# Performance work log

Measured on AMD Instinct MI355X. Metric: run time of the kernel, lower is better.

## Reference

```python
import jax, jax.numpy as jnp
import numpy as np

N_NODES = 50000
N_EDGES = 1600000
IN_DIM = 128
HIDDEN = 256
N_CLASSES = 2
N_GRAPHS = 512
BN_EPS = 1e-5


def setup_inputs() -> dict:
    key = jax.random.key(0)
    ks = jax.random.split(key, 12)
    x = jax.random.normal(ks[0], (N_NODES, IN_DIM), dtype=jnp.float32)
    edge_index = jax.random.randint(ks[1], (2, N_EDGES), 0, N_NODES, dtype=jnp.int64)
    batch = jnp.sort(jax.random.randint(ks[2], (N_NODES,), 0, N_GRAPHS, dtype=jnp.int64))
    s1 = 1.0 / np.sqrt(IN_DIM)
    s2 = 1.0 / np.sqrt(HIDDEN)
    return {
        "x": x,
        "edge_index": edge_index,
        "batch": batch,
        # GIN MLP: Linear(in,hidden) -> BN -> ReLU -> Linear(hidden,hidden)
        "W1": jax.random.uniform(ks[3], (IN_DIM, HIDDEN), jnp.float32, -s1, s1),
        "b1": jnp.zeros((HIDDEN,), jnp.float32),
        "g1": jnp.ones((HIDDEN,), jnp.float32),
        "be1": jnp.zeros((HIDDEN,), jnp.float32),
        "W2": jax.random.uniform(ks[4], (HIDDEN, HIDDEN), jnp.float32, -s2, s2),
        "b2": jnp.zeros((HIDDEN,), jnp.float32),
        # attention gate: Linear(hidden, 1)
        "Wg": jax.random.uniform(ks[5], (HIDDEN, 1), jnp.float32, -s2, s2),
        "bg": jnp.zeros((1,), jnp.float32),
        # head: BN(hidden) -> Dropout(eval: identity) -> Linear(hidden, n_classes)
        "g2": jnp.ones((HIDDEN,), jnp.float32),
        "be2": jnp.zeros((HIDDEN,), jnp.float32),
        "Wh": jax.random.uniform(ks[6], (HIDDEN, N_CLASSES), jnp.float32, -s2, s2),
        "bh": jnp.zeros((N_CLASSES,), jnp.float32),
    }


def _batchnorm(h, gamma, beta):
    # training-mode BN: batch statistics over axis 0 (biased variance, as torch)
    mu = jnp.mean(h, axis=0)
    var = jnp.mean(jnp.square(h - mu), axis=0)
    return gamma * (h - mu) * jax.lax.rsqrt(var + BN_EPS) + beta


def reference(x, edge_index, batch, W1, b1, g1, be1, W2, b2, Wg, bg, g2, be2, Wh, bh):
    src, dst = edge_index[0], edge_index[1]
    # GINConv (eps=0): agg_i = sum_{j->i} x_j ; h = MLP(x + agg)
    agg = jax.ops.segment_sum(x[src], dst, num_segments=N_NODES)  # [N, in_dim]
    h = x + agg
    h = h @ W1 + b1                      # [N, hidden]
    h = jax.nn.relu(_batchnorm(h, g1, be1))
    h = h @ W2 + b2                      # [N, hidden]
    h = jax.nn.relu(h)                   # outer F.relu in forward
    # AttentionalAggregation: segment softmax of gate, weighted sum per graph
    gate = h @ Wg + bg                   # [N, 1]
    m = jax.ops.segment_max(gate, batch, num_segments=N_GRAPHS)  # [G, 1]
    e = jnp.exp(gate - m[batch])
    s = jax.ops.segment_sum(e, batch, num_segments=N_GRAPHS)     # [G, 1]
    alpha = e / s[batch]                 # [N, 1]
    pooled = jax.ops.segment_sum(alpha * h, batch, num_segments=N_GRAPHS)  # [G, hidden]
    # head: BN -> (Dropout eval = identity) -> Linear -> log_softmax
    z = _batchnorm(pooled, g2, be2) @ Wh + bh  # [G, n_classes]
    return jax.nn.log_softmax(z, axis=-1)
```

## Files before the change

kernel.cpp:

```cpp
#include <hip/hip_runtime.h>

typedef unsigned int u32;
typedef unsigned short ushort_t;
typedef __attribute__((ext_vector_type(8))) short bf16x8;
typedef __attribute__((ext_vector_type(4))) float f32x4;

__device__ __forceinline__ float bf2f_lo(u32 u){
  union{u32 i; float f;} v; v.i = u<<16; return v.f;
}
__device__ __forceinline__ float bf2f_hi(u32 u){
  union{u32 i; float f;} v; v.i = u & 0xFFFF0000u; return v.f;
}
__device__ __forceinline__ float bf2f_s(ushort_t u){
  union{u32 i; float f;} v; v.i = ((u32)u)<<16; return v.f;
}
__device__ __forceinline__ u32 pack2bf(float a, float b){
  union{float f; u32 i;} va, vb; va.f=a; vb.f=b;
  u32 ra = (va.i + 0x7FFF + ((va.i>>16)&1)) >> 16;
  u32 rb = (vb.i + 0x7FFF + ((vb.i>>16)&1)) & 0xFFFF0000u;
  return ra | rb;
}
__device__ __forceinline__ ushort_t f2bf1(float f){
  union{float f; u32 i;} v; v.f=f;
  u32 r = v.i + 0x7FFF + ((v.i>>16)&1);
  return (ushort_t)(r>>16);
}

__global__ __launch_bounds__(256) void to_bf16(const float* __restrict__ x, u32* __restrict__ xb, long n4){
  long i = (long)blockIdx.x*256 + threadIdx.x;
  if(i*4 >= n4*4) return;
  float4 v = ((const float4*)x)[i];
  uint2 o; o.x = pack2bf(v.x, v.y); o.y = pack2bf(v.z, v.w);
  ((uint2*)xb)[i] = o;
}

__global__ __launch_bounds__(256) void transpose_w(const float* __restrict__ W, ushort_t* __restrict__ Wt, int K){
  int n = blockIdx.x;
  for(int k = threadIdx.x; k < K; k += 256){
    Wt[(size_t)n*K + k] = f2bf1(W[(size_t)k*256 + n]);
  }
}

__global__ __launch_bounds__(256) void hist_k(const int* __restrict__ dst, int* __restrict__ bcount,
                                              int E, int N, int NB){
  __shared__ int h[1024];
  for(int i=threadIdx.x; i<1024; i+=256) h[i]=0;
  __syncthreads();
  int e0 = blockIdx.x*8192;
  int e1 = min(e0+8192, E);
  for(int i=e0+threadIdx.x; i<e1; i+=256){
    int d = dst[i];
    if((u32)d >= (u32)N) d = 0;
    atomicAdd(&h[d>>6], 1);
  }
  __syncthreads();
  for(int i=threadIdx.x; i<NB; i+=256){
    int v = h[i];
    if(v) atomicAdd(&bcount[i], v);
  }
}

__global__ __launch_bounds__(256) void bucket_scan(const int* __restrict__ bcount, int* __restrict__ bstart,
                                                   int* __restrict__ bcursor, int NB){
  __shared__ int tsum[256];
  int t = threadIdx.x;
  int base = t*4;
  int a0 = (base+0<NB)?bcount[base+0]:0;
  int a1 = (base+1<NB)?bcount[base+1]:0;
  int a2 = (base+2<NB)?bcount[base+2]:0;
  int a3 = (base+3<NB)?bcount[base+3]:0;
  int s0=a0, s1=s0+a1, s2=s1+a2, s3=s2+a3;
  tsum[t]=s3; __syncthreads();
  #pragma unroll
  for(int d=1; d<256; d<<=1){
    int v = (t>=d)?tsum[t-d]:0;
    __syncthreads();
    tsum[t]+=v;
    __syncthreads();
  }
  int prev = (t>0)?tsum[t-1]:0;
  if(base+0<NB){ bstart[base+0]=prev;    bcursor[(base+0)*16]=0; }
  if(base+1<NB){ bstart[base+1]=prev+s0; bcursor[(base+1)*16]=0; }
  if(base+2<NB){ bstart[base+2]=prev+s1; bcursor[(base+2)*16]=0; }
  if(base+3<NB){ bstart[base+3]=prev+s2; bcursor[(base+3)*16]=0; }
  if(t==255){ bstart[NB]=prev+s3; }
}

__global__ __launch_bounds__(256) void binscatter2(const int* __restrict__ src, const int* __restrict__ dst,
                                                   const int* __restrict__ bstart, int* __restrict__ bcursor,
                                                   u32* __restrict__ pairs, int E, int N, int NB){
  __shared__ int hist[1024];
  __shared__ int base[1024];
  int e0 = blockIdx.x*8192;
  int e1 = min(e0+8192, E);
  for(int i=threadIdx.x; i<NB; i+=256) hist[i]=0;
  __syncthreads();
  for(int i=e0+threadIdx.x; i<e1; i+=256){
    int d = dst[i];
    if((u32)d >= (u32)N) d = 0;
    atomicAdd(&hist[d>>6], 1);
  }
  __syncthreads();
  for(int i=threadIdx.x; i<NB; i+=256){
    int c = hist[i];
    base[i] = c ? (bstart[i] + atomicAdd(&bcursor[i*16], c)) : 0;
    hist[i] = 0;
  }
  __syncthreads();
  for(int i=e0+threadIdx.x; i<e1; i+=256){
    int d = dst[i]; if((u32)d >= (u32)N) d = 0;
    int s = src[i]; if((u32)s >= (u32)N) s = 0;
    int b = d>>6;
    int loc = atomicAdd(&hist[b], 1);
    pairs[base[b]+loc] = (u32)s | (((u32)(d & 63))<<17);
  }
}

#define BCAP 4096
__global__ __launch_bounds__(512) void gather_bucket(const u32* __restrict__ xb,
                                                     const u32* __restrict__ pairs,
                                                     const int* __restrict__ bstart,
                                                     u32* __restrict__ h0b, int N){
  __shared__ int lsrc[BCAP];
  __shared__ int dcnt[64];
  __shared__ int dstart[65];
  __shared__ int dcur[64];
  int b = blockIdx.x;
  int p0 = bstart[b], p1 = bstart[b+1];
  int cnt = p1 - p0;
  int tid = threadIdx.x;
  if(tid < 64) dcnt[tid] = 0;
  __syncthreads();
  bool fits = (cnt <= BCAP) && (cnt >= 0);
  if(fits){
    for(int i=tid; i<cnt; i+=512){
      u32 u = pairs[p0+i];
      atomicAdd(&dcnt[(u>>17)&63], 1);
    }
    __syncthreads();
    if(tid==0){
      int run=0;
      #pragma unroll
      for(int j=0;j<64;j++){ dstart[j]=run; dcur[j]=run; run+=dcnt[j]; }
      dstart[64]=run;
    }
    __syncthreads();
    for(int i=tid; i<cnt; i+=512){
      u32 u = pairs[p0+i];
      int pos = atomicAdd(&dcur[(u>>17)&63], 1);
      lsrc[pos] = (int)(u & 0x1FFFFu);
    }
    __syncthreads();
  }
  const uint4* xr = (const uint4*)xb;
  int slot = tid >> 4;
  int c = tid & 15;
  for(int pass=0; pass<2; pass++){
    int r = pass*32 + slot;
    int node = b*64 + r;
    if(node >= N) continue;
    uint4 xv = xr[(size_t)node*16 + c];
    float acc[8] = {
      bf2f_lo(xv.x), bf2f_hi(xv.x), bf2f_lo(xv.y), bf2f_hi(xv.y),
      bf2f_lo(xv.z), bf2f_hi(xv.z), bf2f_lo(xv.w), bf2f_hi(xv.w) };
    if(fits){
      int ds = dstart[r], de = dstart[r+1];
      int j = ds;
      for(; j+8 <= de; j += 8){
        int s0=lsrc[j+0], s1=lsrc[j+1], s2=lsrc[j+2], s3=lsrc[j+3];
        int s4=lsrc[j+4], s5=lsrc[j+5], s6=lsrc[j+6], s7=lsrc[j+7];
        uint4 v0 = xr[(size_t)s0*16 + c];
        uint4 v1 = xr[(size_t)s1*16 + c];
        uint4 v2 = xr[(size_t)s2*16 + c];
        uint4 v3 = xr[(size_t)s3*16 + c];
        uint4 v4 = xr[(size_t)s4*16 + c];
        uint4 v5 = xr[(size_t)s5*16 + c];
        uint4 v6 = xr[(size_t)s6*16 + c];
        uint4 v7 = xr[(size_t)s7*16 + c];
        acc[0]+=bf2f_lo(v0.x)+bf2f_lo(v1.x)+bf2f_lo(v2.x)+bf2f_lo(v3.x)
               +bf2f_lo(v4.x)+bf2f_lo(v5.x)+bf2f_lo(v6.x)+bf2f_lo(v7.x);
        acc[1]+=bf2f_hi(v0.x)+bf2f_hi(v1.x)+bf2f_hi(v2.x)+bf2f_hi(v3.x)
               +bf2f_hi(v4.x)+bf2f_hi(v5.x)+bf2f_hi(v6.x)+bf2f_hi(v7.x);
        acc[2]+=bf2f_lo(v0.y)+bf2f_lo(v1.y)+bf2f_lo(v2.y)+bf2f_lo(v3.y)
               +bf2f_lo(v4.y)+bf2f_lo(v5.y)+bf2f_lo(v6.y)+bf2f_lo(v7.y);
        acc[3]+=bf2f_hi(v0.y)+bf2f_hi(v1.y)+bf2f_hi(v2.y)+bf2f_hi(v3.y)
               +bf2f_hi(v4.y)+bf2f_hi(v5.y)+bf2f_hi(v6.y)+bf2f_hi(v7.y);
        acc[4]+=bf2f_lo(v0.z)+bf2f_lo(v1.z)+bf2f_lo(v2.z)+bf2f_lo(v3.z)
               +bf2f_lo(v4.z)+bf2f_lo(v5.z)+bf2f_lo(v6.z)+bf2f_lo(v7.z);
        acc[5]+=bf2f_hi(v0.z)+bf2f_hi(v1.z)+bf2f_hi(v2.z)+bf2f_hi(v3.z)
               +bf2f_hi(v4.z)+bf2f_hi(v5.z)+bf2f_hi(v6.z)+bf2f_hi(v7.z);
        acc[6]+=bf2f_lo(v0.w)+bf2f_lo(v1.w)+bf2f_lo(v2.w)+bf2f_lo(v3.w)
               +bf2f_lo(v4.w)+bf2f_lo(v5.w)+bf2f_lo(v6.w)+bf2f_lo(v7.w);
        acc[7]+=bf2f_hi(v0.w)+bf2f_hi(v1.w)+bf2f_hi(v2.w)+bf2f_hi(v3.w)
               +bf2f_hi(v4.w)+bf2f_hi(v5.w)+bf2f_hi(v6.w)+bf2f_hi(v7.w);
      }
      for(; j < de; j++){
        int s = lsrc[j];
        uint4 v = xr[(size_t)s*16 + c];
        acc[0]+=bf2f_lo(v.x); acc[1]+=bf2f_hi(v.x);
        acc[2]+=bf2f_lo(v.y); acc[3]+=bf2f_hi(v.y);
        acc[4]+=bf2f_lo(v.z); acc[5]+=bf2f_hi(v.z);
        acc[6]+=bf2f_lo(v.w); acc[7]+=bf2f_hi(v.w);
      }
    } else {
      for(int i=0;i<cnt;i++){
        u32 u = pairs[p0+i];
        if((int)((u>>17)&63) == r){
          int s = (int)(u & 0x1FFFFu);
          uint4 v = xr[(size_t)s*16 + c];
          acc[0]+=bf2f_lo(v.x); acc[1]+=bf2f_hi(v.x);
          acc[2]+=bf2f_lo(v.y); acc[3]+=bf2f_hi(v.y);
          acc[4]+=bf2f_lo(v.z); acc[5]+=bf2f_hi(v.z);
          acc[6]+=bf2f_lo(v.w); acc[7]+=bf2f_hi(v.w);
        }
      }
    }
    uint4 o;
    o.x = pack2bf(acc[0],acc[1]); o.y = pack2bf(acc[2],acc[3]);
    o.z = pack2bf(acc[4],acc[5]); o.w = pack2bf(acc[6],acc[7]);
    ((uint4*)h0b)[(size_t)node*16 + c] = o;
  }
}

template<int K, bool BNA, bool RELUOUT, bool GATE, bool ABF16, bool OUTBF16>
__global__ __launch_bounds__(512) void gemm_mfma(const void* __restrict__ Ap, const ushort_t* __restrict__ Wt,
                                                 const float* __restrict__ bias,
                                                 const float* __restrict__ scale, const float* __restrict__ shift,
                                                 void* __restrict__ Cp, int M,
                                                 const float* __restrict__ Wg, const float* __restrict__ bg,
                                                 float* __restrict__ gate){
  __shared__ uint4 Al[8*129];
  __shared__ uint4 Bl[8*257];
  __shared__ float gacc[128];
  const int tid  = threadIdx.x;
  const int lane = tid & 63;
  const int wave = tid >> 6;
  const int lm   = lane & 15;
  const int q    = lane >> 4;
  const int mhalf= wave >> 2;
  const int nq   = wave & 3;
  const int m0   = blockIdx.x * 128;

  if(GATE && tid < 128) gacc[tid] = 0.f;

  f32x4 acc[4][4];
  #pragma unroll
  for(int i=0;i<4;i++)
    #pragma unroll
    for(int j=0;j<4;j++) acc[i][j] = (f32x4){0.f,0.f,0.f,0.f};

  for(int k0=0; k0<K; k0+=64){
    #pragma unroll
    for(int i=0;i<2;i++){
      int idx = tid*2 + i;
      int m = idx >> 3, c = idx & 7;
      int grow = m0 + m;
      int kk = k0 + c*8;
      uint4 v = make_uint4(0,0,0,0);
      if(ABF16){
        if(grow < M) v = *(const uint4*)((const ushort_t*)Ap + (size_t)grow*K + kk);
        if(BNA){
          float f0=bf2f_lo(v.x), f1=bf2f_hi(v.x), f2=bf2f_lo(v.y), f3=bf2f_hi(v.y);
          float f4=bf2f_lo(v.z), f5=bf2f_hi(v.z), f6=bf2f_lo(v.w), f7=bf2f_hi(v.w);
          float4 s0 = *(const float4*)(scale+kk),  s1 = *(const float4*)(scale+kk+4);
          float4 t0 = *(const float4*)(shift+kk),  t1 = *(const float4*)(shift+kk+4);
          f0=fmaxf(fmaf(s0.x,f0,t0.x),0.f); f1=fmaxf(fmaf(s0.y,f1,t0.y),0.f);
          f2=fmaxf(fmaf(s0.z,f2,t0.z),0.f); f3=fmaxf(fmaf(s0.w,f3,t0.w),0.f);
          f4=fmaxf(fmaf(s1.x,f4,t1.x),0.f); f5=fmaxf(fmaf(s1.y,f5,t1.y),0.f);
          f6=fmaxf(fmaf(s1.z,f6,t1.z),0.f); f7=fmaxf(fmaf(s1.w,f7,t1.w),0.f);
          v.x = pack2bf(f0,f1); v.y = pack2bf(f2,f3);
          v.z = pack2bf(f4,f5); v.w = pack2bf(f6,f7);
        }
      } else {
        float4 u0 = make_float4(0,0,0,0), u1 = make_float4(0,0,0,0);
        if(grow < M){
          u0 = *(const float4*)((const float*)Ap + (size_t)grow*K + kk);
          u1 = *(const float4*)((const float*)Ap + (size_t)grow*K + kk + 4);
        }
        if(BNA){
          float4 s0 = *(const float4*)(scale+kk),  s1 = *(const float4*)(scale+kk+4);
          float4 t0 = *(const float4*)(shift+kk),  t1 = *(const float4*)(shift+kk+4);
          u0.x=fmaxf(fmaf(s0.x,u0.x,t0.x),0.f); u0.y=fmaxf(fmaf(s0.y,u0.y,t0.y),0.f);
          u0.z=fmaxf(fmaf(s0.z,u0.z,t0.z),0.f); u0.w=fmaxf(fmaf(s0.w,u0.w,t0.w),0.f);
          u1.x=fmaxf(fmaf(s1.x,u1.x,t1.x),0.f); u1.y=fmaxf(fmaf(s1.y,u1.y,t1.y),0.f);
          u1.z=fmaxf(fmaf(s1.z,u1.z,t1.z),0.f); u1.w=fmaxf(fmaf(s1.w,u1.w,t1.w),0.f);
        }
        v.x = pack2bf(u0.x,u0.y); v.y = pack2bf(u0.z,u0.w);
        v.z = pack2bf(u1.x,u1.y); v.w = pack2bf(u1.z,u1.w);
      }
      Al[c*129 + m] = v;
    }
    #pragma unroll
    for(int i=0;i<4;i++){
      int idx = tid*4 + i;
      int n = idx >> 3, c = idx & 7;
      Bl[c*257 + n] = *(const uint4*)(Wt + (size_t)n*K + k0 + c*8);
    }
    __syncthreads();
    #pragma unroll
    for(int ks=0; ks<2; ks++){
      int cc = ks*4 + q;
      bf16x8 af[4], bfr[4];
      #pragma unroll
      for(int mi=0; mi<4; mi++)
        af[mi] = *((const bf16x8*)&Al[cc*129 + mhalf*64 + mi*16 + lm]);
      #pragma unroll
      for(int ni=0; ni<4; ni++)
        bfr[ni] = *((const bf16x8*)&Bl[cc*257 + nq*64 + ni*16 + lm]);
      #pragma unroll
      for(int mi=0; mi<4; mi++)
        #pragma unroll
        for(int ni=0; ni<4; ni++)
          acc[mi][ni] = __builtin_amdgcn_mfma_f32_16x16x32_bf16(af[mi], bfr[ni], acc[mi][ni], 0, 0, 0);
    }
    __syncthreads();
  }

  float bb[4], wgv[4];
  #pragma unroll
  for(int ni=0; ni<4; ni++){
    int col = nq*64 + ni*16 + lm;
    bb[ni] = bias[col];
    if(GATE) wgv[ni] = Wg[col];
  }
  #pragma unroll
  for(int mi=0; mi<4; mi++){
    int rowloc0 = mhalf*64 + mi*16 + q*4;
    float gp[4] = {0.f,0.f,0.f,0.f};
    #pragma unroll
    for(int ni=0; ni<4; ni++){
      int col = nq*64 + ni*16 + lm;
      f32x4 o = acc[mi][ni];
      #pragma unroll
      for(int r=0; r<4; r++){
        float v = o[r] + bb[ni];
        if(RELUOUT) v = fmaxf(v, 0.f);
        int row = m0 + rowloc0 + r;
        if(row < M){
          if(OUTBF16) ((ushort_t*)Cp)[(size_t)row*256 + col] = f2bf1(v);
          else        ((float*)Cp)[(size_t)row*256 + col] = v;
        }
        if(GATE) gp[r] = fmaf(v, wgv[ni], gp[r]);
      }
    }
    if(GATE){
      #pragma unroll
      for(int r=0; r<4; r++){
        if(m0 + rowloc0 + r < M) atomicAdd(&gacc[rowloc0 + r], gp[r]);
      }
    }
  }
  if(GATE){
    __syncthreads();
    if(tid < 128){
      int row = m0 + tid;
      if(row < M) gate[row] = gacc[tid] + bg[0];
    }
  }
}

__global__ __launch_bounds__(256) void col_stats_bf(const u32* __restrict__ h, float* __restrict__ psum,
                                                    float* __restrict__ pq, int M, int rpb, int nblk){
  int b = blockIdx.x;
  int g = threadIdx.x >> 6;
  int lane = threadIdx.x & 63;
  int c0 = lane*4;
  int r0 = b*rpb;
  int r1 = min(r0+rpb, M);
  float4 s4 = make_float4(0.f,0.f,0.f,0.f);
  float4 q4 = make_float4(0.f,0.f,0.f,0.f);
  for(int r=r0+g; r<r1; r+=4){
    uint2 u = *(const uint2*)(h + (size_t)r*128 + lane*2);
    float v0=bf2f_lo(u.x), v1=bf2f_hi(u.x), v2=bf2f_lo(u.y), v3=bf2f_hi(u.y);
    s4.x+=v0; s4.y+=v1; s4.z+=v2; s4.w+=v3;
    q4.x=fmaf(v0,v0,q4.x); q4.y=fmaf(v1,v1,q4.y);
    q4.z=fmaf(v2,v2,q4.z); q4.w=fmaf(v3,v3,q4.w);
  }
  __shared__ float ls[1024];
  __shared__ float lq[1024];
  *(float4*)&ls[g*256+c0] = s4;
  *(float4*)&lq[g*256+c0] = q4;
  __syncthreads();
  if(threadIdx.x < 64){
    #pragma unroll
    for(int j=0;j<4;j++){
      int c = c0+j;
      float s = ls[c]+ls[256+c]+ls[512+c]+ls[768+c];
      float q = lq[c]+lq[256+c]+lq[512+c]+lq[768+c];
      psum[(size_t)c*nblk + b] = s;
      pq[(size_t)c*nblk + b]   = q;
    }
  }
}

__global__ __launch_bounds__(256) void col_stats2(const float* __restrict__ h, float* __restrict__ psum,
                                                  float* __restrict__ pq, int M, int rpb, int nblk){
  int b = blockIdx.x;
  int g = threadIdx.x >> 6;
  int lane = threadIdx.x & 63;
  int c0 = lane*4;
  int r0 = b*rpb;
  int r1 = min(r0+rpb, M);
  float4 s4 = make_float4(0.f,0.f,0.f,0.f);
  float4 q4 = make_float4(0.f,0.f,0.f,0.f);
  for(int r=r0+g; r<r1; r+=4){
    float4 v = *(const float4*)(h + (size_t)r*256 + c0);
    s4.x+=v.x; s4.y+=v.y; s4.z+=v.z; s4.w+=v.w;
    q4.x=fmaf(v.x,v.x,q4.x); q4.y=fmaf(v.y,v.y,q4.y);
    q4.z=fmaf(v.z,v.z,q4.z); q4.w=fmaf(v.w,v.w,q4.w);
  }
  __shared__ float ls[1024];
  __shared__ float lq[1024];
  *(float4*)&ls[g*256+c0] = s4;
  *(float4*)&lq[g*256+c0] = q4;
  __syncthreads();
  if(threadIdx.x < 64){
    #pragma unroll
    for(int j=0;j<4;j++){
      int c = c0+j;
      float s = ls[c]+ls[256+c]+ls[512+c]+ls[768+c];
      float q = lq[c]+lq[256+c]+lq[512+c]+lq[768+c];
      psum[(size_t)c*nblk + b] = s;
      pq[(size_t)c*nblk + b]   = q;
    }
  }
}

__global__ __launch_bounds__(512) void stats_fin(const float* __restrict__ psum, const float* __restrict__ pq,
                                                 const float* __restrict__ gamma, const float* __restrict__ beta,
                                                 float* __restrict__ scale, float* __restrict__ shift,
                                                 int nblk, float invM){
  __shared__ float red[512];
  int t = threadIdx.x;
  const float* src = (t<256) ? (psum + (size_t)t*nblk) : (pq + (size_t)(t-256)*nblk);
  float s = 0.f;
  for(int i=0;i<nblk;i+=4){
    float4 v = *(const float4*)(src+i);
    s += v.x+v.y+v.z+v.w;
  }
  red[t]=s; __syncthreads();
  if(t<256){
    float mu  = red[t]*invM;
    float var = fmaxf(red[256+t]*invM - mu*mu, 0.f);
    float sc  = gamma[t] * rsqrtf(var + 1e-5f);
    scale[t]=sc; shift[t]=fmaf(-mu, sc, beta[t]);
  }
}

__global__ __launch_bounds__(512) void pool_k(const ushort_t* __restrict__ h2b, const float* __restrict__ gate,
                                              const int* __restrict__ batch, float* __restrict__ pooled, int N){
  int g = blockIdx.x;
  __shared__ int sb[2];
  __shared__ float red[8];
  __shared__ float s_m, s_inv;
  __shared__ float la[256];
  __shared__ float facc[512];
  int t = threadIdx.x;
  if(t < 2){
    int target = g + t;
    int lo=0, hi=N;
    while(lo<hi){ int mid=(lo+hi)>>1; if(batch[mid] < target) lo=mid+1; else hi=mid; }
    sb[t] = lo;
  }
  __syncthreads();
  int beg = sb[0], end = sb[1];
  float mx = -1e30f;
  for(int i=beg+t; i<end; i+=512) mx = fmaxf(mx, gate[i]);
  #pragma unroll
  for(int d=32; d>0; d>>=1) mx = fmaxf(mx, __shfl_down(mx, d, 64));
  if((t&63)==0) red[t>>6] = mx;
  __syncthreads();
  if(t==0){
    float m = red[0];
    #pragma unroll
    for(int w=1; w<8; w++) m = fmaxf(m, red[w]);
    s_m = m;
  }
  __syncthreads();
  float m = s_m;
  float s = 0.f;
  for(int i=beg+t; i<end; i+=512) s += expf(gate[i]-m);
  #pragma unroll
  for(int d=32; d>0; d>>=1) s += __shfl_down(s, d, 64);
  if((t&63)==0) red[t>>6] = s;
  __syncthreads();
  if(t==0){
    float tot = 0.f;
    #pragma unroll
    for(int w=0; w<8; w++) tot += red[w];
    s_inv = (tot > 0.f) ? 1.f/tot : 0.f;
  }
  __syncthreads();
  float inv = s_inv;
  int col = t & 255;
  int half = t >> 8;
  float acc = 0.f;
  for(int ci=beg; ci<end; ci+=256){
    int chunk = min(256, end-ci);
    if(t < 256) la[t] = (t < chunk) ? expf(gate[ci+t]-m)*inv : 0.f;
    __syncthreads();
    for(int j=half; j<chunk; j+=2){
      acc = fmaf(la[j], bf2f_s(h2b[(size_t)(ci+j)*256 + col]), acc);
    }
    __syncthreads();
  }
  facc[t] = acc;
  __syncthreads();
  if(t < 256) pooled[g*256 + t] = facc[t] + facc[t+256];
}

__global__ __launch_bounds__(256) void head_k(const float* __restrict__ pooled,
                                              const float* __restrict__ sc2, const float* __restrict__ sh2,
                                              const float* __restrict__ Wh, const float* __restrict__ bh,
                                              float* __restrict__ out, int G){
  int w = (blockIdx.x*256 + threadIdx.x) >> 6;
  int l = threadIdx.x & 63;
  if(w >= G) return;
  float4 v  = *(const float4*)(pooled + (size_t)w*256 + l*4);
  float4 sc = *(const float4*)(sc2 + l*4);
  float4 sh = *(const float4*)(sh2 + l*4);
  float vv[4] = { fmaf(sc.x,v.x,sh.x), fmaf(sc.y,v.y,sh.y), fmaf(sc.z,v.z,sh.z), fmaf(sc.w,v.w,sh.w) };
  float4 w0 = *(const float4*)(Wh + (size_t)l*8);
  float4 w1 = *(const float4*)(Wh + (size_t)l*8 + 4);
  float a0 = vv[0]*w0.x + vv[1]*w0.z + vv[2]*w1.x + vv[3]*w1.z;
  float a1 = vv[0]*w0.y + vv[1]*w0.w + vv[2]*w1.y + vv[3]*w1.w;
  #pragma unroll
  for(int d=32; d>0; d>>=1){ a0 += __shfl_down(a0,d,64); a1 += __shfl_down(a1,d,64); }
  if(l==0){
    float z0 = a0 + bh[0];
    float z1 = a1 + bh[1];
    float mz = fmaxf(z0,z1);
    float lse = mz + logf(expf(z0-mz) + expf(z1-mz));
    out[w*2]   = z0 - lse;
    out[w*2+1] = z1 - lse;
  }
}

extern "C" void kernel_launch(void* const* d_in, const int* in_sizes, int n_in,
                              void* d_out, int out_size, void* d_ws, size_t ws_size,
                              hipStream_t stream){
  const float* x   = (const float*)d_in[0];
  const int*   ei  = (const int*)d_in[1];
  const int*   bat = (const int*)d_in[2];
  const float* W1  = (const float*)d_in[3];
  const float* b1  = (const float*)d_in[4];
  const float* g1  = (const float*)d_in[5];
  const float* be1 = (const float*)d_in[6];
  const float* W2  = (const float*)d_in[7];
  const float* b2  = (const float*)d_in[8];
  const float* Wg  = (const float*)d_in[9];
  const float* bg  = (const float*)d_in[10];
  const float* g2  = (const float*)d_in[11];
  const float* be2 = (const float*)d_in[12];
  const float* Wh  = (const float*)d_in[13];
  const float* bh  = (const float*)d_in[14];

  const int N = in_sizes[0] / 128;
  const int E = in_sizes[1] / 2;
  const int G = out_size / 2;
  const int NB = (N + 63) >> 6;
  const int NBLK1 = 512;
  const int NBLK2 = 64;

  char* ws = (char*)d_ws;
  u32*   h0b    = (u32*)ws;
  u32*   xb     = (u32*)(ws + 12800000);
  u32*   pairs  = (u32*)(ws + 25600000);
  int*   bcount = (int*)(ws + 32000000);
  int*   bstart = (int*)(ws + 32004352);
  int*   bcursor= (int*)(ws + 32008704);
  ushort_t* h2b = (ushort_t*)ws;
  u32*   h1b    = (u32*)(ws + 51200000);
  char*  p2 = ws + 102400000;
  float* psum1 = (float*)p2;          p2 += 256*NBLK1*4;
  float* pq1   = (float*)p2;          p2 += 256*NBLK1*4;
  float* psum2 = (float*)p2;          p2 += 256*NBLK2*4;
  float* pq2   = (float*)p2;          p2 += 256*NBLK2*4;
  float* sc1   = (float*)p2;          p2 += 1024;
  float* sh1   = (float*)p2;          p2 += 1024;
  float* gate  = (float*)p2;          p2 += (size_t)N*4 + 4096;
  float* pooled= (float*)p2;          p2 += (size_t)G*256*4;
  float* sc2   = (float*)p2;          p2 += 1024;
  float* sh2   = (float*)p2;          p2 += 1024;
  ushort_t* W1t = (ushort_t*)p2;      p2 += 256*128*2;
  ushort_t* W2t = (ushort_t*)p2;      p2 += 256*256*2;

  const int* src = ei;
  const int* dst = ei + E;

  hipMemsetAsync(bcount, 0, (size_t)NB*4, stream);

  transpose_w<<<256, 256, 0, stream>>>(W1, W1t, 128);
  transpose_w<<<256, 256, 0, stream>>>(W2, W2t, 256);
  long n4 = (long)N*128/4;
  to_bf16    <<<(int)((n4+255)/256), 256, 0, stream>>>(x, xb, n4);

  int nchunk = (E + 8191)/8192;
  hist_k     <<<nchunk, 256, 0, stream>>>(dst, bcount, E, N, NB);
  bucket_scan<<<1, 256, 0, stream>>>(bcount, bstart, bcursor, NB);
  binscatter2<<<nchunk, 256, 0, stream>>>(src, dst, bstart, bcursor, pairs, E, N, NB);
  gather_bucket<<<NB, 512, 0, stream>>>(xb, pairs, bstart, h0b, N);

  int gblocks = (N + 127)/128;
  gemm_mfma<128,false,false,false,true,true><<<gblocks, 512, 0, stream>>>(
      h0b, W1t, b1, nullptr, nullptr, h1b, N, nullptr, nullptr, nullptr);
  int rpb1 = (N + NBLK1 - 1)/NBLK1;
  col_stats_bf <<<NBLK1, 256, 0, stream>>>(h1b, psum1, pq1, N, rpb1, NBLK1);
  stats_fin  <<<1, 512, 0, stream>>>(psum1, pq1, g1, be1, sc1, sh1, NBLK1, 1.0f/(float)N);
  gemm_mfma<256,true,true,true,true,true><<<gblocks, 512, 0, stream>>>(
      h1b, W2t, b2, sc1, sh1, h2b, N, Wg, bg, gate);

  pool_k <<<G, 512, 0, stream>>>(h2b, gate, bat, pooled, N);
  int rpb2 = (G + NBLK2 - 1)/NBLK2;
  col_stats2 <<<NBLK2, 256, 0, stream>>>(pooled, psum2, pq2, G, rpb2, NBLK2);
  stats_fin  <<<1, 512, 0, stream>>>(psum2, pq2, g2, be2, sc2, sh2, NBLK2, 1.0f/(float)G);
  head_k <<<(G+3)/4, 256, 0, stream>>>(pooled, sc2, sh2, Wh, bh, (float*)d_out, G);
}
```

Before: 356.9 us.

## Fuse BN1 column stats into GEMM epilogue, split gather buckets, vectorize pooling

```diff
diff --git a/kernel.cpp b/kernel.cpp
--- a/kernel.cpp
+++ b/kernel.cpp
@@ -116,122 +116,129 @@
   }
 }
 
-#define BCAP 4096
+#define BCAP2 2560
 __global__ __launch_bounds__(512) void gather_bucket(const u32* __restrict__ xb,
                                                      const u32* __restrict__ pairs,
                                                      const int* __restrict__ bstart,
                                                      u32* __restrict__ h0b, int N){
-  __shared__ int lsrc[BCAP];
-  __shared__ int dcnt[64];
-  __shared__ int dstart[65];
-  __shared__ int dcur[64];
-  int b = blockIdx.x;
+  __shared__ int lsrc[BCAP2];
+  __shared__ int dcnt[32];
+  __shared__ int dstart[33];
+  __shared__ int dcur[32];
+  __shared__ int s_fits;
+  int b    = blockIdx.x >> 1;
+  int half = blockIdx.x & 1;
   int p0 = bstart[b], p1 = bstart[b+1];
   int cnt = p1 - p0;
   int tid = threadIdx.x;
-  if(tid < 64) dcnt[tid] = 0;
-  __syncthreads();
-  bool fits = (cnt <= BCAP) && (cnt >= 0);
+  if(tid < 32) dcnt[tid] = 0;
+  __syncthreads();
+  for(int i=tid; i<cnt; i+=512){
+    u32 u = pairs[p0+i];
+    int loc = (u>>17)&63;
+    if((loc>>5) == half) atomicAdd(&dcnt[loc&31], 1);
+  }
+  __syncthreads();
+  if(tid==0){
+    int run=0;
+    #pragma unroll
+    for(int j=0;j<32;j++){ dstart[j]=run; dcur[j]=run; run+=dcnt[j]; }
+    dstart[32]=run;
+    s_fits = (run <= BCAP2) ? 1 : 0;
+  }
+  __syncthreads();
+  bool fits = (s_fits != 0);
   if(fits){
     for(int i=tid; i<cnt; i+=512){
       u32 u = pairs[p0+i];
-      atomicAdd(&dcnt[(u>>17)&63], 1);
-    }
-    __syncthreads();
-    if(tid==0){
-      int run=0;
-      #pragma unroll
-      for(int j=0;j<64;j++){ dstart[j]=run; dcur[j]=run; run+=dcnt[j]; }
-      dstart[64]=run;
-    }
-    __syncthreads();
-    for(int i=tid; i<cnt; i+=512){
-      u32 u = pairs[p0+i];
-      int pos = atomicAdd(&dcur[(u>>17)&63], 1);
-      lsrc[pos] = (int)(u & 0x1FFFFu);
+      int loc = (u>>17)&63;
+      if((loc>>5) == half){
+        int pos = atomicAdd(&dcur[loc&31], 1);
+        lsrc[pos] = (int)(u & 0x1FFFFu);
+      }
     }
     __syncthreads();
   }
   const uint4* xr = (const uint4*)xb;
   int slot = tid >> 4;
   int c = tid & 15;
-  for(int pass=0; pass<2; pass++){
-    int r = pass*32 + slot;
-    int node = b*64 + r;
-    if(node >= N) continue;
-    uint4 xv = xr[(size_t)node*16 + c];
-    float acc[8] = {
-      bf2f_lo(xv.x), bf2f_hi(xv.x), bf2f_lo(xv.y), bf2f_hi(xv.y),
-      bf2f_lo(xv.z), bf2f_hi(xv.z), bf2f_lo(xv.w), bf2f_hi(xv.w) };
-    if(fits){
-      int ds = dstart[r], de = dstart[r+1];
-      int j = ds;
-      for(; j+8 <= de; j += 8){
-        int s0=lsrc[j+0], s1=lsrc[j+1], s2=lsrc[j+2], s3=lsrc[j+3];
-        int s4=lsrc[j+4], s5=lsrc[j+5], s6=lsrc[j+6], s7=lsrc[j+7];
-        uint4 v0 = xr[(size_t)s0*16 + c];
-        uint4 v1 = xr[(size_t)s1*16 + c];
-        uint4 v2 = xr[(size_t)s2*16 + c];
-        uint4 v3 = xr[(size_t)s3*16 + c];
-        uint4 v4 = xr[(size_t)s4*16 + c];
-        uint4 v5 = xr[(size_t)s5*16 + c];
-        uint4 v6 = xr[(size_t)s6*16 + c];
-        uint4 v7 = xr[(size_t)s7*16 + c];
-        acc[0]+=bf2f_lo(v0.x)+bf2f_lo(v1.x)+bf2f_lo(v2.x)+bf2f_lo(v3.x)
-               +bf2f_lo(v4.x)+bf2f_lo(v5.x)+bf2f_lo(v6.x)+bf2f_lo(v7.x);
-        acc[1]+=bf2f_hi(v0.x)+bf2f_hi(v1.x)+bf2f_hi(v2.x)+bf2f_hi(v3.x)
-               +bf2f_hi(v4.x)+bf2f_hi(v5.x)+bf2f_hi(v6.x)+bf2f_hi(v7.x);
-        acc[2]+=bf2f_lo(v0.y)+bf2f_lo(v1.y)+bf2f_lo(v2.y)+bf2f_lo(v3.y)
-               +bf2f_lo(v4.y)+bf2f_lo(v5.y)+bf2f_lo(v6.y)+bf2f_lo(v7.y);
-        acc[3]+=bf2f_hi(v0.y)+bf2f_hi(v1.y)+bf2f_hi(v2.y)+bf2f_hi(v3.y)
-               +bf2f_hi(v4.y)+bf2f_hi(v5.y)+bf2f_hi(v6.y)+bf2f_hi(v7.y);
-        acc[4]+=bf2f_lo(v0.z)+bf2f_lo(v1.z)+bf2f_lo(v2.z)+bf2f_lo(v3.z)
-               +bf2f_lo(v4.z)+bf2f_lo(v5.z)+bf2f_lo(v6.z)+bf2f_lo(v7.z);
-        acc[5]+=bf2f_hi(v0.z)+bf2f_hi(v1.z)+bf2f_hi(v2.z)+bf2f_hi(v3.z)
-               +bf2f_hi(v4.z)+bf2f_hi(v5.z)+bf2f_hi(v6.z)+bf2f_hi(v7.z);
-        acc[6]+=bf2f_lo(v0.w)+bf2f_lo(v1.w)+bf2f_lo(v2.w)+bf2f_lo(v3.w)
-               +bf2f_lo(v4.w)+bf2f_lo(v5.w)+bf2f_lo(v6.w)+bf2f_lo(v7.w);
-        acc[7]+=bf2f_hi(v0.w)+bf2f_hi(v1.w)+bf2f_hi(v2.w)+bf2f_hi(v3.w)
-               +bf2f_hi(v4.w)+bf2f_hi(v5.w)+bf2f_hi(v6.w)+bf2f_hi(v7.w);
-      }
-      for(; j < de; j++){
-        int s = lsrc[j];
+  int node = b*64 + half*32 + slot;
+  if(node >= N) return;
+  uint4 xv = xr[(size_t)node*16 + c];
+  float acc[8] = {
+    bf2f_lo(xv.x), bf2f_hi(xv.x), bf2f_lo(xv.y), bf2f_hi(xv.y),
+    bf2f_lo(xv.z), bf2f_hi(xv.z), bf2f_lo(xv.w), bf2f_hi(xv.w) };
+  if(fits){
+    int ds = dstart[slot], de = dstart[slot+1];
+    int j = ds;
+    for(; j+8 <= de; j += 8){
+      int s0=lsrc[j+0], s1=lsrc[j+1], s2=lsrc[j+2], s3=lsrc[j+3];
+      int s4=lsrc[j+4], s5=lsrc[j+5], s6=lsrc[j+6], s7=lsrc[j+7];
+      uint4 v0 = xr[(size_t)s0*16 + c];
+      uint4 v1 = xr[(size_t)s1*16 + c];
+      uint4 v2 = xr[(size_t)s2*16 + c];
+      uint4 v3 = xr[(size_t)s3*16 + c];
+      uint4 v4 = xr[(size_t)s4*16 + c];
+      uint4 v5 = xr[(size_t)s5*16 + c];
+      uint4 v6 = xr[(size_t)s6*16 + c];
+      uint4 v7 = xr[(size_t)s7*16 + c];
+      acc[0]+=bf2f_lo(v0.x)+bf2f_lo(v1.x)+bf2f_lo(v2.x)+bf2f_lo(v3.x)
+             +bf2f_lo(v4.x)+bf2f_lo(v5.x)+bf2f_lo(v6.x)+bf2f_lo(v7.x);
+      acc[1]+=bf2f_hi(v0.x)+bf2f_hi(v1.x)+bf2f_hi(v2.x)+bf2f_hi(v3.x)
+             +bf2f_hi(v4.x)+bf2f_hi(v5.x)+bf2f_hi(v6.x)+bf2f_hi(v7.x);
+      acc[2]+=bf2f_lo(v0.y)+bf2f_lo(v1.y)+bf2f_lo(v2.y)+bf2f_lo(v3.y)
+             +bf2f_lo(v4.y)+bf2f_lo(v5.y)+bf2f_lo(v6.y)+bf2f_lo(v7.y);
+      acc[3]+=bf2f_hi(v0.y)+bf2f_hi(v1.y)+bf2f_hi(v2.y)+bf2f_hi(v3.y)
+             +bf2f_hi(v4.y)+bf2f_hi(v5.y)+bf2f_hi(v6.y)+bf2f_hi(v7.y);
+      acc[4]+=bf2f_lo(v0.z)+bf2f_lo(v1.z)+bf2f_lo(v2.z)+bf2f_lo(v3.z)
+             +bf2f_lo(v4.z)+bf2f_lo(v5.z)+bf2f_lo(v6.z)+bf2f_lo(v7.z);
+      acc[5]+=bf2f_hi(v0.z)+bf2f_hi(v1.z)+bf2f_hi(v2.z)+bf2f_hi(v3.z)
+             +bf2f_hi(v4.z)+bf2f_hi(v5.z)+bf2f_hi(v6.z)+bf2f_hi(v7.z);
+      acc[6]+=bf2f_lo(v0.w)+bf2f_lo(v1.w)+bf2f_lo(v2.w)+bf2f_lo(v3.w)
+             +bf2f_lo(v4.w)+bf2f_lo(v5.w)+bf2f_lo(v6.w)+bf2f_lo(v7.w);
+      acc[7]+=bf2f_hi(v0.w)+bf2f_hi(v1.w)+bf2f_hi(v2.w)+bf2f_hi(v3.w)
+             +bf2f_hi(v4.w)+bf2f_hi(v5.w)+bf2f_hi(v6.w)+bf2f_hi(v7.w);
+    }
+    for(; j < de; j++){
+      int s = lsrc[j];
+      uint4 v = xr[(size_t)s*16 + c];
+      acc[0]+=bf2f_lo(v.x); acc[1]+=bf2f_hi(v.x);
+      acc[2]+=bf2f_lo(v.y); acc[3]+=bf2f_hi(v.y);
+      acc[4]+=bf2f_lo(v.z); acc[5]+=bf2f_hi(v.z);
+      acc[6]+=bf2f_lo(v.w); acc[7]+=bf2f_hi(v.w);
+    }
+  } else {
+    int want = half*32 + slot;
+    for(int i=0;i<cnt;i++){
+      u32 u = pairs[p0+i];
+      if((int)((u>>17)&63) == want){
+        int s = (int)(u & 0x1FFFFu);
         uint4 v = xr[(size_t)s*16 + c];
         acc[0]+=bf2f_lo(v.x); acc[1]+=bf2f_hi(v.x);
         acc[2]+=bf2f_lo(v.y); acc[3]+=bf2f_hi(v.y);
         acc[4]+=bf2f_lo(v.z); acc[5]+=bf2f_hi(v.z);
         acc[6]+=bf2f_lo(v.w); acc[7]+=bf2f_hi(v.w);
       }
-    } else {
-      for(int i=0;i<cnt;i++){
-        u32 u = pairs[p0+i];
-        if((int)((u>>17)&63) == r){
-          int s = (int)(u & 0x1FFFFu);
-          uint4 v = xr[(size_t)s*16 + c];
-          acc[0]+=bf2f_lo(v.x); acc[1]+=bf2f_hi(v.x);
-          acc[2]+=bf2f_lo(v.y); acc[3]+=bf2f_hi(v.y);
-          acc[4]+=bf2f_lo(v.z); acc[5]+=bf2f_hi(v.z);
-          acc[6]+=bf2f_lo(v.w); acc[7]+=bf2f_hi(v.w);
-        }
-      }
-    }
-    uint4 o;
-    o.x = pack2bf(acc[0],acc[1]); o.y = pack2bf(acc[2],acc[3]);
-    o.z = pack2bf(acc[4],acc[5]); o.w = pack2bf(acc[6],acc[7]);
-    ((uint4*)h0b)[(size_t)node*16 + c] = o;
-  }
-}
-
-template<int K, bool BNA, bool RELUOUT, bool GATE, bool ABF16, bool OUTBF16>
+    }
+  }
+  uint4 o;
+  o.x = pack2bf(acc[0],acc[1]); o.y = pack2bf(acc[2],acc[3]);
+  o.z = pack2bf(acc[4],acc[5]); o.w = pack2bf(acc[6],acc[7]);
+  ((uint4*)h0b)[(size_t)node*16 + c] = o;
+}
+
+template<int K, bool BNA, bool RELUOUT, bool GATE, bool ABF16, bool OUTBF16, bool STATS>
 __global__ __launch_bounds__(512) void gemm_mfma(const void* __restrict__ Ap, const ushort_t* __restrict__ Wt,
                                                  const float* __restrict__ bias,
                                                  const float* __restrict__ scale, const float* __restrict__ shift,
                                                  void* __restrict__ Cp, int M,
                                                  const float* __restrict__ Wg, const float* __restrict__ bg,
-                                                 float* __restrict__ gate){
+                                                 float* __restrict__ gate,
+                                                 float* __restrict__ psum, float* __restrict__ pq, int NS){
   __shared__ uint4 Al[8*129];
   __shared__ uint4 Bl[8*257];
   __shared__ float gacc[128];
+  __shared__ float sstat[512];
   const int tid  = threadIdx.x;
   const int lane = tid & 63;
   const int wave = tid >> 6;
@@ -242,6 +249,7 @@
   const int m0   = blockIdx.x * 128;
 
   if(GATE && tid < 128) gacc[tid] = 0.f;
+  if(STATS){ sstat[tid] = 0.f; }
 
   f32x4 acc[4][4];
   #pragma unroll
@@ -317,6 +325,8 @@
   }
 
   float bb[4], wgv[4];
+  float cs[4] = {0.f,0.f,0.f,0.f};
+  float cq[4] = {0.f,0.f,0.f,0.f};
   #pragma unroll
   for(int ni=0; ni<4; ni++){
     int col = nq*64 + ni*16 + lm;
@@ -339,6 +349,7 @@
         if(row < M){
           if(OUTBF16) ((ushort_t*)Cp)[(size_t)row*256 + col] = f2bf1(v);
           else        ((float*)Cp)[(size_t)row*256 + col] = v;
+          if(STATS){ cs[ni] += v; cq[ni] = fmaf(v, v, cq[ni]); }
         }
         if(GATE) gp[r] = fmaf(v, wgv[ni], gp[r]);
       }
@@ -350,45 +361,25 @@
       }
     }
   }
+  if(STATS){
+    __syncthreads();
+    #pragma unroll
+    for(int ni=0; ni<4; ni++){
+      int col = nq*64 + ni*16 + lm;
+      atomicAdd(&sstat[col], cs[ni]);
+      atomicAdd(&sstat[256+col], cq[ni]);
+    }
+    __syncthreads();
+    if(tid < 256){
+      psum[(size_t)tid*NS + blockIdx.x] = sstat[tid];
+      pq[(size_t)tid*NS + blockIdx.x]   = sstat[256+tid];
+    }
+  }
   if(GATE){
     __syncthreads();
     if(tid < 128){
       int row = m0 + tid;
       if(row < M) gate[row] = gacc[tid] + bg[0];
-    }
-  }
-}
-
-__global__ __launch_bounds__(256) void col_stats_bf(const u32* __restrict__ h, float* __restrict__ psum,
-                                                    float* __restrict__ pq, int M, int rpb, int nblk){
-  int b = blockIdx.x;
-  int g = threadIdx.x >> 6;
-  int lane = threadIdx.x & 63;
-  int c0 = lane*4;
-  int r0 = b*rpb;
-  int r1 = min(r0+rpb, M);
-  float4 s4 = make_float4(0.f,0.f,0.f,0.f);
-  float4 q4 = make_float4(0.f,0.f,0.f,0.f);
-  for(int r=r0+g; r<r1; r+=4){
-    uint2 u = *(const uint2*)(h + (size_t)r*128 + lane*2);
-    float v0=bf2f_lo(u.x), v1=bf2f_hi(u.x), v2=bf2f_lo(u.y), v3=bf2f_hi(u.y);
-    s4.x+=v0; s4.y+=v1; s4.z+=v2; s4.w+=v3;
-    q4.x=fmaf(v0,v0,q4.x); q4.y=fmaf(v1,v1,q4.y);
-    q4.z=fmaf(v2,v2,q4.z); q4.w=fmaf(v3,v3,q4.w);
-  }
-  __shared__ float ls[1024];
-  __shared__ float lq[1024];
-  *(float4*)&ls[g*256+c0] = s4;
-  *(float4*)&lq[g*256+c0] = q4;
-  __syncthreads();
-  if(threadIdx.x < 64){
-    #pragma unroll
-    for(int j=0;j<4;j++){
-      int c = c0+j;
-      float s = ls[c]+ls[256+c]+ls[512+c]+ls[768+c];
-      float q = lq[c]+lq[256+c]+lq[512+c]+lq[768+c];
-      psum[(size_t)c*nblk + b] = s;
-      pq[(size_t)c*nblk + b]   = q;
     }
   }
 }
@@ -454,7 +445,8 @@
   __shared__ float red[8];
   __shared__ float s_m, s_inv;
   __shared__ float la[256];
-  __shared__ float facc[512];
+  __shared__ float sa0[512];
+  __shared__ float sa1[512];
   int t = threadIdx.x;
   if(t < 2){
     int target = g + t;
@@ -492,21 +484,30 @@
   }
   __syncthreads();
   float inv = s_inv;
-  int col = t & 255;
-  int half = t >> 8;
-  float acc = 0.f;
+  const u32* h2w = (const u32*)h2b;
+  int colpair = t & 127;
+  int rowgrp  = t >> 7;
+  float a0 = 0.f, a1 = 0.f;
   for(int ci=beg; ci<end; ci+=256){
     int chunk = min(256, end-ci);
     if(t < 256) la[t] = (t < chunk) ? expf(gate[ci+t]-m)*inv : 0.f;
     __syncthreads();
-    for(int j=half; j<chunk; j+=2){
-      acc = fmaf(la[j], bf2f_s(h2b[(size_t)(ci+j)*256 + col]), acc);
-    }
-    __syncthreads();
-  }
-  facc[t] = acc;
-  __syncthreads();
-  if(t < 256) pooled[g*256 + t] = facc[t] + facc[t+256];
+    for(int j=rowgrp; j<chunk; j+=4){
+      u32 h = h2w[(size_t)(ci+j)*128 + colpair];
+      float w = la[j];
+      a0 = fmaf(w, bf2f_lo(h), a0);
+      a1 = fmaf(w, bf2f_hi(h), a1);
+    }
+    __syncthreads();
+  }
+  sa0[t] = a0; sa1[t] = a1;
+  __syncthreads();
+  if(t < 128){
+    float r0 = sa0[t] + sa0[128+t] + sa0[256+t] + sa0[384+t];
+    float r1 = sa1[t] + sa1[128+t] + sa1[256+t] + sa1[384+t];
+    pooled[g*256 + t*2]   = r0;
+    pooled[g*256 + t*2+1] = r1;
+  }
 }
 
 __global__ __launch_bounds__(256) void head_k(const float* __restrict__ pooled,
@@ -559,7 +560,7 @@
   const int E = in_sizes[1] / 2;
   const int G = out_size / 2;
   const int NB = (N + 63) >> 6;
-  const int NBLK1 = 512;
+  const int NS1 = 512;
   const int NBLK2 = 64;
 
   char* ws = (char*)d_ws;
@@ -572,8 +573,8 @@
   ushort_t* h2b = (ushort_t*)ws;
   u32*   h1b    = (u32*)(ws + 51200000);
   char*  p2 = ws + 102400000;
-  float* psum1 = (float*)p2;          p2 += 256*NBLK1*4;
-  float* pq1   = (float*)p2;          p2 += 256*NBLK1*4;
+  float* psum1 = (float*)p2;          p2 += 256*NS1*4;
+  float* pq1   = (float*)p2;          p2 += 256*NS1*4;
   float* psum2 = (float*)p2;          p2 += 256*NBLK2*4;
   float* pq2   = (float*)p2;          p2 += 256*NBLK2*4;
   float* sc1   = (float*)p2;          p2 += 1024;
@@ -589,6 +590,8 @@
   const int* dst = ei + E;
 
   hipMemsetAsync(bcount, 0, (size_t)NB*4, stream);
+  hipMemsetAsync(psum1, 0, (size_t)256*NS1*4, stream);
+  hipMemsetAsync(pq1,   0, (size_t)256*NS1*4, stream);
 
   transpose_w<<<256, 256, 0, stream>>>(W1, W1t, 128);
   transpose_w<<<256, 256, 0, stream>>>(W2, W2t, 256);
@@ -599,16 +602,14 @@
   hist_k     <<<nchunk, 256, 0, stream>>>(dst, bcount, E, N, NB);
   bucket_scan<<<1, 256, 0, stream>>>(bcount, bstart, bcursor, NB);
   binscatter2<<<nchunk, 256, 0, stream>>>(src, dst, bstart, bcursor, pairs, E, N, NB);
-  gather_bucket<<<NB, 512, 0, stream>>>(xb, pairs, bstart, h0b, N);
+  gather_bucket<<<NB*2, 512, 0, stream>>>(xb, pairs, bstart, h0b, N);
 
   int gblocks = (N + 127)/128;
-  gemm_mfma<128,false,false,false,true,true><<<gblocks, 512, 0, stream>>>(
-      h0b, W1t, b1, nullptr, nullptr, h1b, N, nullptr, nullptr, nullptr);
-  int rpb1 = (N + NBLK1 - 1)/NBLK1;
-  col_stats_bf <<<NBLK1, 256, 0, stream>>>(h1b, psum1, pq1, N, rpb1, NBLK1);
-  stats_fin  <<<1, 512, 0, stream>>>(psum1, pq1, g1, be1, sc1, sh1, NBLK1, 1.0f/(float)N);
-  gemm_mfma<256,true,true,true,true,true><<<gblocks, 512, 0, stream>>>(
-      h1b, W2t, b2, sc1, sh1, h2b, N, Wg, bg, gate);
+  gemm_mfma<128,false,false,false,true,true,true><<<gblocks, 512, 0, stream>>>(
+      h0b, W1t, b1, nullptr, nullptr, h1b, N, nullptr, nullptr, nullptr, psum1, pq1, NS1);
+  stats_fin  <<<1, 512, 0, stream>>>(psum1, pq1, g1, be1, sc1, sh1, NS1, 1.0f/(float)N);
+  gemm_mfma<256,true,true,true,true,true,false><<<gblocks, 512, 0, stream>>>(
+      h1b, W2t, b2, sc1, sh1, h2b, N, Wg, bg, gate, nullptr, nullptr, 0);
 
   pool_k <<<G, 512, 0, stream>>>(h2b, gate, bat, pooled, N);
   int rpb2 = (G + NBLK2 - 1)/NBLK2;
```

Result: no change. 353.8 us (-0.9%).
